# Kernel optimization log

Measured on AMD Instinct MI355X. Metric: run time of the kernel, lower is better.

## Reference

```python
import jax, jax.numpy as jnp
import numpy as np

B, T, N, H, L, KS = 8, 1024, 64, 8, 2, 3  # batch, seq_len, num_features(=graph n), heads, blocks, Cheb order
D1 = 64  # tq MLP hidden (hardcoded 64 in original)
EPS = 1e-6


def setup_inputs() -> dict:
    key = jax.random.key(0)
    ks = jax.random.split(key, 30)
    def nrm(k, shp, sc=0.05):
        return jax.random.normal(k, shp, dtype=jnp.float32) * sc
    return {
        "inputs": jax.random.normal(ks[0], (B, T, N), dtype=jnp.float32),
        "pos_emb": nrm(ks[1], (T, N)),
        "K3": nrm(ks[2], (N, KS, N), 0.1),  # Chebyshev kernel Lk reshaped [n, Ks, n] (constant)
        "qw": nrm(ks[3], (L, H, KS)), "qb": nrm(ks[4], (L, H)),
        "kw": nrm(ks[5], (L, H, KS)), "kb": nrm(ks[6], (L, H)),
        "vw": nrm(ks[7], (L, H, KS)), "vb": nrm(ks[8], (L, H)),
        "tqW1": nrm(ks[9], (L, H, T, D1)), "tqb1": nrm(ks[10], (L, H, D1)),
        "tqW2": nrm(ks[11], (L, H, D1, D1)), "tqb2": nrm(ks[12], (L, H, D1)),
        "tqW3": nrm(ks[13], (L, H, D1, 2)), "tqb3": nrm(ks[14], (L, H, 2)),
        "Wlt": nrm(ks[15], (L, H * N, N)),
        "ln1g": jnp.ones((L, N), jnp.float32), "ln1b": jnp.zeros((L, N), jnp.float32),
        "ln2g": jnp.ones((L, N), jnp.float32), "ln2b": jnp.zeros((L, N), jnp.float32),
        "sclw": nrm(ks[16], (L, KS)), "sclb": nrm(ks[17], (L,)),
        "elW": nrm(ks[18], (L, N, N)), "elb": nrm(ks[19], (L, N)),
        "fW1": nrm(ks[20], (N, 32)), "fb1": nrm(ks[21], (32,)),
        "fW2": nrm(ks[22], (32, 1)), "fb2": nrm(ks[23], (1,)),
    }


def _ln(x, g, b):
    m = jnp.mean(x, axis=-1, keepdims=True)
    v = jnp.mean((x - m) ** 2, axis=-1, keepdims=True)
    return (x - m) * jax.lax.rsqrt(v + EPS) * g + b


def _head_gconv(x, K3, ws, bs):
    # SpatialConvLayer (c_in=c_out=1) per head: relu(sum_k ws[h,k]*(x @ L_k) + bs[h] + x)
    g = jnp.einsum('btn,nkm,hk->bhtm', x, K3, ws) + bs[None, :, None, None]
    return jax.nn.relu(g + x[:, None])  # [B,H,T,N]


def reference(inputs, pos_emb, K3, qw, qb, kw, kb, vw, vb, tqW1, tqb1, tqW2, tqb2,
              tqW3, tqb3, Wlt, ln1g, ln1b, ln2g, ln2b, sclw, sclb, elW, elb,
              fW1, fb1, fW2, fb2):
    x = inputs + pos_emb  # position embedding layer
    for l in range(L):
        xq = _head_gconv(x, K3, qw[l], qb[l])
        xk = _head_gconv(x, K3, kw[l], kb[l])
        xv = _head_gconv(x, K3, vw[l], vb[l])
        # s_a[b,t,s] = sum_n xk[b,t,n] * xq[b,s,n], scaled by 1/num_features
        s = jnp.einsum('bhtn,bhsn->bhts', xk, xq) / N
        sft = jax.nn.softmax(s, axis=-1)
        # talking-quantity gate: MLP over rows of transposed softmax matrix
        p = jnp.swapaxes(sft, -1, -2)  # [B,H,T,T]
        h1 = jax.nn.relu(jnp.einsum('bhts,hsd->bhtd', p, tqW1[l]) + tqb1[l][None, :, None, :])
        h2 = jax.nn.relu(jnp.einsum('bhtd,hde->bhte', h1, tqW2[l]) + tqb2[l][None, :, None, :])
        g = jax.nn.softmax(jnp.einsum('bhtd,hde->bhte', h2, tqW3[l]) + tqb3[l][None, :, None, :], axis=-1)  # [B,H,T,2]
        auv = jnp.einsum('bhts,bhsn->bhtn', sft, xv)
        ho = g[..., 0:1] * auv + g[..., 1:2] * xv  # gated mix, [B,H,T,N]
        a_x = jnp.transpose(ho, (0, 2, 1, 3)).reshape(B, T, H * N)  # head concat
        out1 = _ln(x + a_x @ Wlt[l], ln1g[l], ln1b[l])  # dropout omitted (inference)
        gc = jnp.einsum('btn,nkm,k->btm', out1, K3, sclw[l]) + sclb[l]
        ffn = jax.nn.relu(gc + out1)  # SpatialConvLayer residual relu
        ffn = ffn @ elW[l] + elb[l]
        x = _ln(out1 + ffn, ln2g[l], ln2b[l])
    pooled = jnp.mean(x, axis=1)  # GlobalAveragePooling1D
    h = jax.nn.relu(pooled @ fW1 + fb1)
    return h @ fW2 + fb2  # [B,1]
```

## Files before the change

kernel.cpp:

```cpp
#include <hip/hip_runtime.h>

typedef __attribute__((ext_vector_type(8))) short short8;
typedef __attribute__((ext_vector_type(4))) float f32x4;

#define BB 8
#define TT 1024
#define NN 64
#define HH 8
#define LL 2
#define KSS 3
#define DD1 64
#define EPSV 1e-6f
#define LOG2E 1.4426950408889634f

#define MFMA16(a, b, c) __builtin_amdgcn_mfma_f32_16x16x32_bf16(a, b, c, 0, 0, 0)
#define BAR() __builtin_amdgcn_s_barrier()
#define WAIT_VM8() asm volatile("s_waitcnt vmcnt(8)" ::: "memory")
#define WAIT_VM2() asm volatile("s_waitcnt vmcnt(2)" ::: "memory")
#define WAIT_VM0() asm volatile("s_waitcnt vmcnt(0)" ::: "memory")
#define WAIT_LGKM0() asm volatile("s_waitcnt lgkmcnt(0)" ::: "memory")

__device__ __forceinline__ float exp2_(float x) { return __builtin_amdgcn_exp2f(x); }
__device__ __forceinline__ float log2_(float x) { return __builtin_amdgcn_logf(x); }

__device__ __forceinline__ void split1(float x, ushort& hi, ushort& lo) {
  uint u = __float_as_uint(x);
  hi = (ushort)(u >> 16);
  float hf = __uint_as_float(u & 0xffff0000u);
  lo = (ushort)(__float_as_uint(x - hf) >> 16);
}
__device__ __forceinline__ uint pack2(float a, float b, uint& lo) {
  uint ua = __float_as_uint(a), ub = __float_as_uint(b);
  float ra = __uint_as_float(ua & 0xffff0000u);
  float rb = __uint_as_float(ub & 0xffff0000u);
  lo = (__float_as_uint(a - ra) >> 16) | (__float_as_uint(b - rb) & 0xffff0000u);
  return (ua >> 16) | (ub & 0xffff0000u);
}
__device__ __forceinline__ uint pack2rhu(float a, float b) {
  uint ua = __float_as_uint(a) + 0x8000u;
  uint ub = __float_as_uint(b) + 0x8000u;
  return (ua >> 16) | (ub & 0xffff0000u);
}
__device__ __forceinline__ ushort f2bfr(float x) {
  union { float f; uint u; } v; v.f = x;
  uint r = (v.u + 0x7fffu + ((v.u >> 16) & 1u)) >> 16;
  return (ushort)r;
}
__device__ __forceinline__ float bf2f(ushort b) {
  union { uint u; float f; } v; v.u = ((uint)b) << 16; return v.f;
}

__device__ __forceinline__ void gl2lds16(const ushort* g, ushort* l) {
  __builtin_amdgcn_global_load_lds(
      (const __attribute__((address_space(1))) void*)g,
      (__attribute__((address_space(3))) void*)l, 16, 0, 0);
}
__device__ __forceinline__ void stage_async(ushort* __restrict__ s,
                                            const ushort* __restrict__ g,
                                            int stride, int tid) {
  int w = tid >> 6;
  int sub = (tid & 63) >> 3, c = tid & 7;
#pragma unroll
  for (int i = 0; i < 2; ++i) {
    int rb = (i * 4 + w) * 8;
    gl2lds16(g + (size_t)(rb + sub) * stride + ((c ^ sub) << 3), s + rb * 64);
  }
}
__device__ __forceinline__ short8 frag(const ushort* __restrict__ s, int row, int ch) {
  return *(const short8*)(s + row * 64 + ((ch ^ (row & 7)) << 3));
}
__device__ __forceinline__ void stage_q32(ushort* __restrict__ s,
                                          const ushort* __restrict__ g, int tid) {
  int w = tid >> 6;
  int sub = (tid & 63) >> 3, c = tid & 7;
  int rb = w * 8, r = rb + sub;
  gl2lds16(g + (size_t)r * 64 + ((c ^ (r & 7)) << 3), s + rb * 64);
}
__device__ __forceinline__ void stage_v32(ushort* __restrict__ s,
                                          const ushort* __restrict__ g, int tid) {
  int w = tid >> 6;
  int noff = (tid & 63) >> 2, c = tid & 3;
  int nb = w * 16, n = nb + noff;
  gl2lds16(g + (size_t)n * 1024 + ((c ^ ((n >> 1) & 3)) << 3), s + nb * 32);
}
__device__ __forceinline__ short8 frag32(const ushort* __restrict__ s, int row, int g) {
  return *(const short8*)(s + row * 32 + ((g ^ ((row >> 1) & 3)) << 3));
}


__global__ void k_addpos(const float* __restrict__ in, const float* __restrict__ pe,
                         float* __restrict__ x, int total) {
  int idx = blockIdx.x * 256 + threadIdx.x;
  if (idx < total) {
    int tn = idx & (TT * NN - 1);
    x[idx] = in[idx] + pe[tn];
  }
}

__global__ void k_k3s(const float* __restrict__ K3, const float* __restrict__ sclwl,
                      ushort* __restrict__ dh) {
  int idx = blockIdx.x * 256 + threadIdx.x;
  int n = idx >> 6, m = idx & 63;
  float v = K3[n * 192 + m] * sclwl[0] + K3[n * 192 + 64 + m] * sclwl[1] +
            K3[n * 192 + 128 + m] * sclwl[2];
  dh[m * 64 + n] = f2bfr(v);
}

__global__ __launch_bounds__(256) void k_tsplit(const float* __restrict__ src,
                                                ushort* __restrict__ dh) {
  __shared__ float st[64][65];
  int blk = blockIdx.x;
  int mat = blk >> 4, rt = blk & 15;
  int tid = threadIdx.x;
  size_t sbase = ((size_t)mat * TT + rt * 64) * 64;
#pragma unroll
  for (int i = 0; i < 4; ++i) {
    int idx = tid + i * 256;
    int r = idx >> 4, c4 = idx & 15;
    float4 v = *(const float4*)(src + sbase + r * 64 + c4 * 4);
    st[r][c4 * 4 + 0] = v.x; st[r][c4 * 4 + 1] = v.y;
    st[r][c4 * 4 + 2] = v.z; st[r][c4 * 4 + 3] = v.w;
  }
  __syncthreads();
  size_t obase = (size_t)mat * (64 * (size_t)TT) + rt * 64;
#pragma unroll
  for (int i = 0; i < 2; ++i) {
    int idx = tid + i * 256;
    int n = idx >> 3, c = idx & 7;
    uint hw[4];
#pragma unroll
    for (int j = 0; j < 4; ++j)
      hw[j] = (uint)f2bfr(st[c * 8 + 2 * j][n]) | ((uint)f2bfr(st[c * 8 + 2 * j + 1][n]) << 16);
    *(uint4*)(dh + obase + (size_t)n * TT + c * 8) = make_uint4(hw[0], hw[1], hw[2], hw[3]);
  }
}

__global__ __launch_bounds__(256) void k_tsplitW(const float* __restrict__ Wlt,
                                                 ushort* __restrict__ dh,
                                                 ushort* __restrict__ dl) {
  __shared__ float st[64][65];
  int blk = blockIdx.x;
  int l = blk >> 3, rt = blk & 7;
  int tid = threadIdx.x;
  size_t sbase = ((size_t)l * 512 + rt * 64) * 64;
#pragma unroll
  for (int i = 0; i < 4; ++i) {
    int idx = tid + i * 256;
    int r = idx >> 4, c4 = idx & 15;
    float4 v = *(const float4*)(Wlt + sbase + r * 64 + c4 * 4);
    st[r][c4 * 4 + 0] = v.x; st[r][c4 * 4 + 1] = v.y;
    st[r][c4 * 4 + 2] = v.z; st[r][c4 * 4 + 3] = v.w;
  }
  __syncthreads();
  size_t obase = (size_t)l * 64 * 512 + rt * 64;
#pragma unroll
  for (int i = 0; i < 2; ++i) {
    int idx = tid + i * 256;
    int n = idx >> 3, c = idx & 7;
    uint hw[4], lw[4];
#pragma unroll
    for (int j = 0; j < 4; ++j) hw[j] = pack2(st[c * 8 + 2 * j][n], st[c * 8 + 2 * j + 1][n], lw[j]);
    *(uint4*)(dh + obase + (size_t)n * 512 + c * 8) = make_uint4(hw[0], hw[1], hw[2], hw[3]);
    *(uint4*)(dl + obase + (size_t)n * 512 + c * 8) = make_uint4(lw[0], lw[1], lw[2], lw[3]);
  }
}

__global__ __launch_bounds__(256) void k_tsplitSq(const float* __restrict__ src,
                                                  ushort* __restrict__ dh) {
  __shared__ float st[64][65];
  int mat = blockIdx.x;
  int tid = threadIdx.x;
  size_t sbase = (size_t)mat * 4096;
#pragma unroll
  for (int i = 0; i < 4; ++i) {
    int idx = tid + i * 256;
    int r = idx >> 4, c4 = idx & 15;
    float4 v = *(const float4*)(src + sbase + r * 64 + c4 * 4);
    st[r][c4 * 4 + 0] = v.x; st[r][c4 * 4 + 1] = v.y;
    st[r][c4 * 4 + 2] = v.z; st[r][c4 * 4 + 3] = v.w;
  }
  __syncthreads();
#pragma unroll
  for (int i = 0; i < 2; ++i) {
    int idx = tid + i * 256;
    int d = idx >> 3, c = idx & 7;
    uint hw[4];
#pragma unroll
    for (int j = 0; j < 4; ++j)
      hw[j] = (uint)f2bfr(st[c * 8 + 2 * j][d]) | ((uint)f2bfr(st[c * 8 + 2 * j + 1][d]) << 16);
    *(uint4*)(dh + sbase + (size_t)d * 64 + c * 8) = make_uint4(hw[0], hw[1], hw[2], hw[3]);
  }
}

__global__ __launch_bounds__(256) void k_gconv(
    const float* __restrict__ x, const float* __restrict__ K3,
    const float* __restrict__ qwl, const float* __restrict__ qbl,
    const float* __restrict__ kwl, const float* __restrict__ kbl,
    const float* __restrict__ vwl, const float* __restrict__ vbl,
    ushort* __restrict__ xqh, ushort* __restrict__ xkh, float* __restrict__ xv) {
  __shared__ float sK3[12288];
  __shared__ float sx[4][64];
  int tid = threadIdx.x;
  int w = tid >> 6, lane = tid & 63;
#pragma unroll
  for (int i = 0; i < 12; ++i)
    ((float4*)sK3)[tid + i * 256] = ((const float4*)K3)[tid + i * 256];
  size_t bt = (size_t)blockIdx.x * 4 + w;
  size_t b = bt >> 10, t = bt & 1023;
  float xm = x[bt * 64 + lane];
  sx[w][lane] = xm;
  __syncthreads();
  float a0 = 0.f, a1 = 0.f, a2 = 0.f;
#pragma unroll 8
  for (int n = 0; n < 64; ++n) {
    float xn = sx[w][n];
    a0 = fmaf(xn, sK3[n * 192 + lane], a0);
    a1 = fmaf(xn, sK3[n * 192 + 64 + lane], a1);
    a2 = fmaf(xn, sK3[n * 192 + 128 + lane], a2);
  }
#pragma unroll
  for (int hh = 0; hh < HH; ++hh) {
    size_t off = (((size_t)b * HH + hh) * TT + t) * 64 + lane;
    float q = fmaf(qwl[hh * 3 + 0], a0,
              fmaf(qwl[hh * 3 + 1], a1, fmaf(qwl[hh * 3 + 2], a2, qbl[hh] + xm)));
    q = fmaxf(q, 0.f) * (0.015625f * LOG2E);
    xqh[off] = f2bfr(q);
    float k = fmaf(kwl[hh * 3 + 0], a0,
              fmaf(kwl[hh * 3 + 1], a1, fmaf(kwl[hh * 3 + 2], a2, kbl[hh] + xm)));
    xkh[off] = f2bfr(fmaxf(k, 0.f));
    float v = fmaf(vwl[hh * 3 + 0], a0,
              fmaf(vwl[hh * 3 + 1], a1, fmaf(vwl[hh * 3 + 2], a2, vbl[hh] + xm)));
    xv[off] = fmaxf(v, 0.f);
  }
}

__global__ __launch_bounds__(256, 4) void k_attn(
    const ushort* __restrict__ xkh, const ushort* __restrict__ xqh,
    const ushort* __restrict__ xvTh,
    float* __restrict__ auv, float* __restrict__ lse) {
  __shared__ ushort sQh[4096];
  __shared__ ushort sVh[4096];
  __shared__ ushort sPh[2048];
  int tid = threadIdx.x;
  int lane = tid & 63, w = tid >> 6;
  int l15 = lane & 15, g = lane >> 4;
  int nb = gridDim.x, chunk = nb >> 3, bid = blockIdx.x;
  int blk = (bid & 7) * chunk + (bid >> 3);
  int bh = blk >> 4, t0 = (blk & 15) << 6;
  size_t bhTT = (size_t)bh * TT;
  int trow = 16 * w + l15, psw = (trow >> 1) & 3;

  stage_async(sQh, xkh + (bhTT + t0) * NN, 64, tid);
  WAIT_VM0();
  BAR();
  short8 fKh[2];
#pragma unroll
  for (int ks = 0; ks < 2; ++ks) fKh[ks] = frag(sQh, trow, g + 4 * ks);
  WAIT_LGKM0();
  BAR();
  stage_q32(sQh, xqh + bhTT * NN, tid);
  stage_v32(sVh, xvTh + bhTT * NN, tid);
  stage_q32(sQh + 2048, xqh + (bhTT + 32) * NN, tid);
  stage_v32(sVh + 2048, xvTh + bhTT * NN + 32, tid);

  float lsum = 0.f;
  f32x4 O[4];
#pragma unroll
  for (int ct = 0; ct < 4; ++ct)
#pragma unroll
    for (int r = 0; r < 4; ++r) O[ct][r] = 0.f;

  for (int ut = 0; ut < 32; ++ut) {
    int cur = ut & 1;
    if (ut < 31) WAIT_VM2(); else WAIT_VM0();
    BAR();
    const ushort* cQh = sQh + cur * 2048;
    const ushort* cVh = sVh + cur * 2048;

    __builtin_amdgcn_s_setprio(1);
    f32x4 S[2];
#pragma unroll
    for (int rt = 0; rt < 2; ++rt) {
      f32x4 a = {0.f, 0.f, 0.f, 0.f};
#pragma unroll
      for (int ks = 0; ks < 2; ++ks)
        a = MFMA16(frag(cQh, 16 * rt + l15, g + 4 * ks), fKh[ks], a);
      S[rt] = a;
    }
    __builtin_amdgcn_s_setprio(0);

    uint2 ph[2];
#pragma unroll
    for (int rt = 0; rt < 2; ++rt) {
      float p0 = exp2_(S[rt][0]), p1 = exp2_(S[rt][1]);
      float p2 = exp2_(S[rt][2]), p3 = exp2_(S[rt][3]);
      lsum += (p0 + p1) + (p2 + p3);
      ph[rt].x = pack2rhu(p0, p1);
      ph[rt].y = pack2rhu(p2, p3);
    }
#pragma unroll
    for (int rt = 0; rt < 2; ++rt) {
      int ch = 2 * rt + (g >> 1);
      int off = trow * 32 + ((ch ^ psw) << 3) + ((g & 1) << 2);
      *(uint2*)(sPh + off) = ph[rt];
    }
    WAIT_LGKM0();
    __builtin_amdgcn_sched_barrier(0);
    __builtin_amdgcn_s_setprio(1);
    {
      short8 aPh = frag32(sPh, trow, g);
#pragma unroll
      for (int ct = 0; ct < 4; ++ct)
        O[ct] = MFMA16(aPh, frag32(cVh, 16 * ct + l15, g), O[ct]);
    }
    __builtin_amdgcn_s_setprio(0);
    WAIT_LGKM0();
    BAR();
    if (ut < 30) {
      int tn = ut + 2;
      stage_q32(sQh + cur * 2048, xqh + (bhTT + tn * 32) * NN, tid);
      stage_v32(sVh + cur * 2048, xvTh + bhTT * NN + tn * 32, tid);
    }
  }
  lsum += __shfl_xor(lsum, 16, 64);
  lsum += __shfl_xor(lsum, 32, 64);
  float il = 1.0f / lsum;
  float ilr[4];
#pragma unroll
  for (int r = 0; r < 4; ++r) ilr[r] = __shfl(il, (lane & 48) | (4 * g + r), 64);
#pragma unroll
  for (int r = 0; r < 4; ++r) {
    size_t row = (bhTT + t0 + 16 * w + 4 * g + r) * NN;
#pragma unroll
    for (int ct = 0; ct < 4; ++ct) auv[row + 16 * ct + l15] = O[ct][r] * ilr[r];
  }
  if (g == 0) lse[bhTT + t0 + trow] = log2_(lsum);
}

__global__ __launch_bounds__(256, 4) void k_h1(
    const ushort* __restrict__ xkh, const ushort* __restrict__ xqh,
    const ushort* __restrict__ w1Th,
    const float* __restrict__ lse, const float* __restrict__ b1,
    ushort* __restrict__ h1h) {
  __shared__ ushort sKh[4096];
  __shared__ ushort sWh[4096];
  __shared__ ushort sPh[2048];
  __shared__ float sL[1024];
  int tid = threadIdx.x;
  int lane = tid & 63, w = tid >> 6;
  int l15 = lane & 15, g = lane >> 4;
  int nb = gridDim.x, chunk = nb >> 3, bid = blockIdx.x;
  int blk = (bid & 7) * chunk + (bid >> 3);
  int bh = blk >> 4, h = bh & (HH - 1), a0 = (blk & 15) << 6;
  size_t bhTT = (size_t)bh * TT;
  size_t wbase = (size_t)h * NN * TT;
  int arow = 16 * w + l15, psw = (arow >> 1) & 3;

  stage_async(sKh, xqh + (bhTT + a0) * NN, 64, tid);
  WAIT_VM0();
  BAR();
  short8 fQh[2];
#pragma unroll
  for (int ks = 0; ks < 2; ++ks) fQh[ks] = frag(sKh, arow, g + 4 * ks);
#pragma unroll
  for (int i = 0; i < 4; ++i) sL[tid + i * 256] = lse[bhTT + tid + i * 256];
  WAIT_LGKM0();
  BAR();
  stage_q32(sKh, xkh + bhTT * NN, tid);
  stage_v32(sWh, w1Th + wbase, tid);
  stage_q32(sKh + 2048, xkh + (bhTT + 32) * NN, tid);
  stage_v32(sWh + 2048, w1Th + wbase + 32, tid);

  f32x4 acc[4];
#pragma unroll
  for (int ct = 0; ct < 4; ++ct)
#pragma unroll
    for (int r = 0; r < 4; ++r) acc[ct][r] = 0.f;

  for (int tt = 0; tt < 32; ++tt) {
    int cur = tt & 1;
    if (tt < 31) WAIT_VM2(); else WAIT_VM0();
    BAR();
    const ushort* cKh = sKh + cur * 2048;
    const ushort* cWh = sWh + cur * 2048;

    __builtin_amdgcn_s_setprio(1);
    f32x4 S[2];
#pragma unroll
    for (int rt = 0; rt < 2; ++rt) {
      f32x4 a = {0.f, 0.f, 0.f, 0.f};
#pragma unroll
      for (int ks = 0; ks < 2; ++ks)
        a = MFMA16(frag(cKh, 16 * rt + l15, g + 4 * ks), fQh[ks], a);
      S[rt] = a;
    }
    __builtin_amdgcn_s_setprio(0);

    uint2 ph[2];
#pragma unroll
    for (int rt = 0; rt < 2; ++rt) {
      f32x4 lv = *(const f32x4*)(sL + tt * 32 + 16 * rt + 4 * g);
      float p0 = exp2_(S[rt][0] - lv[0]);
      float p1 = exp2_(S[rt][1] - lv[1]);
      float p2 = exp2_(S[rt][2] - lv[2]);
      float p3 = exp2_(S[rt][3] - lv[3]);
      ph[rt].x = pack2rhu(p0, p1);
      ph[rt].y = pack2rhu(p2, p3);
    }
#pragma unroll
    for (int rt = 0; rt < 2; ++rt) {
      int ch = 2 * rt + (g >> 1);
      int off = arow * 32 + ((ch ^ psw) << 3) + ((g & 1) << 2);
      *(uint2*)(sPh + off) = ph[rt];
    }
    WAIT_LGKM0();
    __builtin_amdgcn_sched_barrier(0);
    __builtin_amdgcn_s_setprio(1);
    {
      short8 aPh = frag32(sPh, arow, g);
#pragma unroll
      for (int ct = 0; ct < 4; ++ct)
        acc[ct] = MFMA16(aPh, frag32(cWh, 16 * ct + l15, g), acc[ct]);
    }
    __builtin_amdgcn_s_setprio(0);
    WAIT_LGKM0();
    BAR();
    if (tt < 30) {
      int tn = tt + 2;
      stage_q32(sKh + cur * 2048, xkh + (bhTT + tn * 32) * NN, tid);
      stage_v32(sWh + cur * 2048, w1Th + wbase + tn * 32, tid);
    }
  }
#pragma unroll
  for (int ct = 0; ct < 4; ++ct) {
    float bb = b1[h * 64 + 16 * ct + l15];
#pragma unroll
    for (int r = 0; r < 4; ++r)
      h1h[(bhTT + a0 + 16 * w + 4 * g + r) * NN + 16 * ct + l15] =
          f2bfr(fmaxf(acc[ct][r] + bb, 0.f));
  }
}

__global__ __launch_bounds__(256) void k_gate(
    const ushort* __restrict__ h1h, const float* __restrict__ xv,
    const ushort* __restrict__ w2Th, const float* __restrict__ b2l,
    const float* __restrict__ W3l, const float* __restrict__ b3l,
    const float* __restrict__ auv, ushort* __restrict__ hoh,
    ushort* __restrict__ hol) {
  __shared__ ushort sA[4096], sB[4096];
  __shared__ float sred[2][64][4];
  __shared__ float sg[64][2];
  int tid = threadIdx.x;
  int lane = tid & 63, w = tid >> 6;
  int l15 = lane & 15, g = lane >> 4;
  int blk = blockIdx.x;
  int bh = blk >> 4, t0 = (blk & 15) << 6, h = bh & (HH - 1);
  size_t bhTT = (size_t)bh * TT;
  stage_async(sA, h1h + (bhTT + t0) * NN, 64, tid);
  stage_async(sB, w2Th + (size_t)h * 4096, 64, tid);
  WAIT_VM0();
  BAR();
  f32x4 acc[4];
#pragma unroll
  for (int rt = 0; rt < 4; ++rt)
#pragma unroll
    for (int r = 0; r < 4; ++r) acc[rt][r] = 0.f;
#pragma unroll
  for (int ks = 0; ks < 2; ++ks) {
    short8 bB = frag(sB, 16 * w + l15, g + 4 * ks);
#pragma unroll
    for (int rt = 0; rt < 4; ++rt)
      acc[rt] = MFMA16(frag(sA, 16 * rt + l15, g + 4 * ks), bB, acc[rt]);
  }
  int col = 16 * w + l15;
  float b2c = b2l[h * 64 + col];
  float w30 = W3l[h * 128 + col * 2 + 0];
  float w31 = W3l[h * 128 + col * 2 + 1];
#pragma unroll
  for (int rt = 0; rt < 4; ++rt)
#pragma unroll
    for (int r = 0; r < 4; ++r) {
      float v = fmaxf(acc[rt][r] + b2c, 0.f);
      float z0 = v * w30, z1 = v * w31;
#pragma unroll
      for (int mm = 1; mm < 16; mm <<= 1) {
        z0 += __shfl_xor(z0, mm, 64);
        z1 += __shfl_xor(z1, mm, 64);
      }
      if (l15 == 0) {
        int row = 16 * rt + 4 * g + r;
        sred[0][row][w] = z0;
        sred[1][row][w] = z1;
      }
    }
  __syncthreads();
  if (tid < 64) {
    float z0 = sred[0][tid][0] + sred[0][tid][1] + sred[0][tid][2] + sred[0][tid][3] +
               b3l[h * 2 + 0];
    float z1 = sred[1][tid][0] + sred[1][tid][1] + sred[1][tid][2] + sred[1][tid][3] +
               b3l[h * 2 + 1];
    float g0 = 1.0f / (1.0f + __expf(z1 - z0));
    sg[tid][0] = g0;
    sg[tid][1] = 1.0f - g0;
  }
  __syncthreads();
#pragma unroll
  for (int rr = 0; rr < 16; ++rr) {
    int row = 16 * w + rr;
    size_t off = (bhTT + t0 + row) * 64 + lane;
    float ho = sg[row][0] * auv[off] + sg[row][1] * xv[off];
    ushort hb, lb;
    split1(ho, hb, lb);
    hoh[off] = hb;
    hol[off] = lb;
  }
}

__global__ __launch_bounds__(256, 2) void k_merge(
    const float* __restrict__ x, const ushort* __restrict__ hoh,
    const ushort* __restrict__ hol, const ushort* __restrict__ wth,
    const ushort* __restrict__ wtl, const float* __restrict__ g1l,
    const float* __restrict__ b1l, ushort* __restrict__ out1h,
    ushort* __restrict__ out1l) {
  __shared__ ushort sAh[2][4096], sAl[2][4096], sBh[2][4096], sBl[2][4096];
  __shared__ float sred[2][64][4];
  __shared__ float sfin[64][2];
  int tid = threadIdx.x;
  int lane = tid & 63, w = tid >> 6;
  int l15 = lane & 15, g = lane >> 4;
  int blk = blockIdx.x;
  int b = blk >> 4, t0 = (blk & 15) << 6;

  {
    size_t ab0 = (((size_t)b * HH + 0) * TT + t0) * NN;
    size_t ab1 = (((size_t)b * HH + 1) * TT + t0) * NN;
    stage_async(sAh[0], hoh + ab0, 64, tid);
    stage_async(sAl[0], hol + ab0, 64, tid);
    stage_async(sBh[0], wth, 512, tid);
    stage_async(sBl[0], wtl, 512, tid);
    stage_async(sAh[1], hoh + ab1, 64, tid);
    stage_async(sAl[1], hol + ab1, 64, tid);
    stage_async(sBh[1], wth + 64, 512, tid);
    stage_async(sBl[1], wtl + 64, 512, tid);
  }

  f32x4 acc[4];
#pragma unroll
  for (int rt = 0; rt < 4; ++rt)
#pragma unroll
    for (int r = 0; r < 4; ++r) acc[rt][r] = 0.f;

  for (int h = 0; h < 8; ++h) {
    int cur = h & 1;
    if (h < 7) WAIT_VM8(); else WAIT_VM0();
    BAR();
    __builtin_amdgcn_s_setprio(1);
#pragma unroll
    for (int ks = 0; ks < 2; ++ks) {
      short8 bBh = frag(sBh[cur], 16 * w + l15, g + 4 * ks);
      short8 bBl = frag(sBl[cur], 16 * w + l15, g + 4 * ks);
#pragma unroll
      for (int rt = 0; rt < 4; ++rt) {
        short8 aAh = frag(sAh[cur], 16 * rt + l15, g + 4 * ks);
        short8 aAl = frag(sAl[cur], 16 * rt + l15, g + 4 * ks);
        acc[rt] = MFMA16(aAh, bBh, acc[rt]);
        acc[rt] = MFMA16(aAh, bBl, acc[rt]);
        acc[rt] = MFMA16(aAl, bBh, acc[rt]);
      }
    }
    __builtin_amdgcn_s_setprio(0);
    WAIT_LGKM0();
    BAR();
    if (h < 6) {
      int hn = h + 2;
      size_t ab = (((size_t)b * HH + hn) * TT + t0) * NN;
      stage_async(sAh[cur], hoh + ab, 64, tid);
      stage_async(sAl[cur], hol + ab, 64, tid);
      stage_async(sBh[cur], wth + hn * 64, 512, tid);
      stage_async(sBl[cur], wtl + hn * 64, 512, tid);
    }
  }
  int mcol = 16 * w + l15;
  float vv[4][4];
#pragma unroll
  for (int rt = 0; rt < 4; ++rt)
#pragma unroll
    for (int r = 0; r < 4; ++r) {
      int row = 16 * rt + 4 * g + r;
      vv[rt][r] = acc[rt][r] + x[((size_t)b * TT + t0 + row) * 64 + mcol];
    }
#pragma unroll
  for (int rt = 0; rt < 4; ++rt)
#pragma unroll
    for (int r = 0; r < 4; ++r) {
      float s1 = vv[rt][r], s2 = vv[rt][r] * vv[rt][r];
#pragma unroll
      for (int mm = 1; mm < 16; mm <<= 1) {
        s1 += __shfl_xor(s1, mm, 64);
        s2 += __shfl_xor(s2, mm, 64);
      }
      if (l15 == 0) {
        int row = 16 * rt + 4 * g + r;
        sred[0][row][w] = s1;
        sred[1][row][w] = s2;
      }
    }
  __syncthreads();
  if (tid < 64) {
    float a1 = sred[0][tid][0] + sred[0][tid][1] + sred[0][tid][2] + sred[0][tid][3];
    float a2 = sred[1][tid][0] + sred[1][tid][1] + sred[1][tid][2] + sred[1][tid][3];
    float mean = a1 * (1.0f / 64.0f);
    float var = a2 * (1.0f / 64.0f) - mean * mean;
    sfin[tid][0] = mean;
    sfin[tid][1] = rsqrtf(var + EPSV);
  }
  __syncthreads();
  float gg = g1l[mcol], bb = b1l[mcol];
#pragma unroll
  for (int rt = 0; rt < 4; ++rt)
#pragma unroll
    for (int r = 0; r < 4; ++r) {
      int row = 16 * rt + 4 * g + r;
      float mean = sfin[row][0], rstd = sfin[row][1];
      float val = (vv[rt][r] - mean) * rstd * gg + bb;
      ushort hb, lb;
      split1(val, hb, lb);
      size_t idx = ((size_t)b * TT + t0 + row) * 64 + mcol;
      out1h[idx] = hb;
      out1l[idx] = lb;
    }
}

__global__ __launch_bounds__(256) void k_ffn(
    const ushort* __restrict__ o1h_, const ushort* __restrict__ o1l_,
    const float* __restrict__ sclb_l, const ushort* __restrict__ k3sTh,
    const ushort* __restrict__ elWTh, const float* __restrict__ elbl,
    const float* __restrict__ g2l, const float* __restrict__ b2l,
    float* __restrict__ xout) {
  __shared__ ushort sAh[2048], sAl[2048];
  __shared__ ushort sB1[4096], sB2[4096];
  __shared__ float sred[2][32][4];
  __shared__ float sfin[32][2];
  int tid = threadIdx.x;
  int lane = tid & 63, w = tid >> 6;
  int l15 = lane & 15, g = lane >> 4;
  int blk = blockIdx.x;
  int b = blk >> 5, t0 = (blk & 31) << 5;
  size_t rb = ((size_t)b * TT + t0) * 64;

  stage_q32(sAh, o1h_ + rb, tid);
  stage_q32(sAl, o1l_ + rb, tid);
  stage_async(sB1, k3sTh, 64, tid);
  stage_async(sB2, elWTh, 64, tid);
  WAIT_VM0();
  BAR();

  int col = 16 * w + l15;
  f32x4 acc[2];
#pragma unroll
  for (int rt = 0; rt < 2; ++rt)
#pragma unroll
    for (int r = 0; r < 4; ++r) acc[rt][r] = 0.f;
#pragma unroll
  for (int ks = 0; ks < 2; ++ks) {
    short8 bB = frag(sB1, col, g + 4 * ks);
#pragma unroll
    for (int rt = 0; rt < 2; ++rt) {
      acc[rt] = MFMA16(frag(sAh, 16 * rt + l15, g + 4 * ks), bB, acc[rt]);
      acc[rt] = MFMA16(frag(sAl, 16 * rt + l15, g + 4 * ks), bB, acc[rt]);
    }
  }
  float sclb = sclb_l[0];
  int cch = col >> 3, cin = col & 7;
  float o1v[2][4], f1v[2][4];
#pragma unroll
  for (int rt = 0; rt < 2; ++rt)
#pragma unroll
    for (int r = 0; r < 4; ++r) {
      int row = 16 * rt + 4 * g + r;
      int a = row * 64 + (((cch ^ (row & 7)) << 3)) + cin;
      float o1 = bf2f(sAh[a]) + bf2f(sAl[a]);
      o1v[rt][r] = o1;
      f1v[rt][r] = fmaxf(acc[rt][r] + sclb + o1, 0.f);
    }
  __syncthreads();
#pragma unroll
  for (int rt = 0; rt < 2; ++rt)
#pragma unroll
    for (int r = 0; r < 4; ++r) {
      int row = 16 * rt + 4 * g + r;
      int a = row * 64 + (((cch ^ (row & 7)) << 3)) + cin;
      ushort hb, lb;
      split1(f1v[rt][r], hb, lb);
      sAh[a] = hb;
      sAl[a] = lb;
    }
  __syncthreads();
  f32x4 acc2[2];
#pragma unroll
  for (int rt = 0; rt < 2; ++rt)
#pragma unroll
    for (int r = 0; r < 4; ++r) acc2[rt][r] = 0.f;
#pragma unroll
  for (int ks = 0; ks < 2; ++ks) {
    short8 bB = frag(sB2, col, g + 4 * ks);
#pragma unroll
    for (int rt = 0; rt < 2; ++rt) {
      acc2[rt] = MFMA16(frag(sAh, 16 * rt + l15, g + 4 * ks), bB, acc2[rt]);
      acc2[rt] = MFMA16(frag(sAl, 16 * rt + l15, g + 4 * ks), bB, acc2[rt]);
    }
  }
  float elb = elbl[col];
  float vv[2][4];
#pragma unroll
  for (int rt = 0; rt < 2; ++rt)
#pragma unroll
    for (int r = 0; r < 4; ++r) {
      vv[rt][r] = o1v[rt][r] + acc2[rt][r] + elb;
      float s1 = vv[rt][r], s2 = vv[rt][r] * vv[rt][r];
#pragma unroll
      for (int mm = 1; mm < 16; mm <<= 1) {
        s1 += __shfl_xor(s1, mm, 64);
        s2 += __shfl_xor(s2, mm, 64);
      }
      if (l15 == 0) {
        int row = 16 * rt + 4 * g + r;
        sred[0][row][w] = s1;
        sred[1][row][w] = s2;
      }
    }
  __syncthreads();
  if (tid < 32) {
    float a1 = sred[0][tid][0] + sred[0][tid][1] + sred[0][tid][2] + sred[0][tid][3];
    float a2 = sred[1][tid][0] + sred[1][tid][1] + sred[1][tid][2] + sred[1][tid][3];
    float mean = a1 * (1.0f / 64.0f);
    float var = a2 * (1.0f / 64.0f) - mean * mean;
    sfin[tid][0] = mean;
    sfin[tid][1] = rsqrtf(var + EPSV);
  }
  __syncthreads();
  float gg = g2l[col], bb = b2l[col];
#pragma unroll
  for (int rt = 0; rt < 2; ++rt)
#pragma unroll
    for (int r = 0; r < 4; ++r) {
      int row = 16 * rt + 4 * g + r;
      xout[rb + (size_t)row * 64 + col] =
          (vv[rt][r] - sfin[row][0]) * sfin[row][1] * gg + bb;
    }
}

__global__ __launch_bounds__(256) void k_final(
    const float* __restrict__ x, const float* __restrict__ fW1,
    const float* __restrict__ fb1, const float* __restrict__ fW2,
    const float* __restrict__ fb2, float* __restrict__ out) {
  __shared__ float pl[4][64];
  int tid = threadIdx.x;
  int lane = tid & 63, w = tid >> 6;
  size_t b = blockIdx.x;
  float s = 0.f;
  for (int t = 256 * w; t < 256 * w + 256; ++t) s += x[(b * TT + t) * 64 + lane];
  pl[w][lane] = s;
  __syncthreads();
  if (tid < 64) pl[0][tid] = (pl[0][tid] + pl[1][tid] + pl[2][tid] + pl[3][tid]) * (1.0f / TT);
  __syncthreads();
  if (tid < 64) {
    float hv = 0.f;
    if (lane < 32) {
      hv = fb1[lane];
#pragma unroll 8
      for (int n = 0; n < 64; ++n) hv = fmaf(pl[0][n], fW1[n * 32 + lane], hv);
      hv = fmaxf(hv, 0.f) * fW2[lane];
    }
#pragma unroll
    for (int m = 1; m < 64; m <<= 1) hv += __shfl_xor(hv, m, 64);
    if (lane == 0) out[b] = hv + fb2[0];
  }
}

extern "C" void kernel_launch(void* const* d_in, const int* in_sizes, int n_in,
                              void* d_out, int out_size, void* d_ws, size_t ws_size,
                              hipStream_t stream) {
  const float* inputs = (const float*)d_in[0];
  const float* pos_emb = (const float*)d_in[1];
  const float* K3 = (const float*)d_in[2];
  const float* qw = (const float*)d_in[3];
  const float* qb = (const float*)d_in[4];
  const float* kw = (const float*)d_in[5];
  const float* kb = (const float*)d_in[6];
  const float* vw = (const float*)d_in[7];
  const float* vb = (const float*)d_in[8];
  const float* tqW1 = (const float*)d_in[9];
  const float* tqb1 = (const float*)d_in[10];
  const float* tqW2 = (const float*)d_in[11];
  const float* tqb2 = (const float*)d_in[12];
  const float* tqW3 = (const float*)d_in[13];
  const float* tqb3 = (const float*)d_in[14];
  const float* Wlt = (const float*)d_in[15];
  const float* ln1g = (const float*)d_in[16];
  const float* ln1b = (const float*)d_in[17];
  const float* ln2g = (const float*)d_in[18];
  const float* ln2b = (const float*)d_in[19];
  const float* sclw = (const float*)d_in[20];
  const float* sclb = (const float*)d_in[21];
  const float* elW = (const float*)d_in[22];
  const float* elb = (const float*)d_in[23];
  const float* fW1 = (const float*)d_in[24];
  const float* fb1 = (const float*)d_in[25];
  const float* fW2 = (const float*)d_in[26];
  const float* fb2 = (const float*)d_in[27];
  float* out = (float*)d_out;
  float* ws_f = (float*)d_ws;

  const size_t TN = (size_t)TT * NN;
  const size_t HTN = (size_t)HH * TT * NN;
  const size_t W1T_ELEMS = (size_t)LL * HH * NN * TT;
  const size_t WLT_ELEMS = (size_t)LL * 64 * 512;

  ushort* k3sTh = (ushort*)ws_f;
  ushort* w1Th = k3sTh + (size_t)LL * 4096;
  ushort* wth = w1Th + W1T_ELEMS;
  ushort* wtl = wth + WLT_ELEMS;
  ushort* w2Th = wtl + WLT_ELEMS;
  ushort* elWTh = w2Th + (size_t)LL * HH * 4096;
  size_t base_ush = (size_t)LL * 4096 + W1T_ELEMS + 2 * WLT_ELEMS +
                    (size_t)LL * HH * 4096 + (size_t)LL * 4096;
  const size_t base = (base_ush + 1) / 2;

  for (int l = 0; l < LL; ++l)
    k_k3s<<<16, 256, 0, stream>>>(K3, sclw + l * KSS, k3sTh + (size_t)l * 4096);
  k_tsplit<<<LL * HH * 16, 256, 0, stream>>>(tqW1, w1Th);
  k_tsplitW<<<LL * 8, 256, 0, stream>>>(Wlt, wth, wtl);
  k_tsplitSq<<<LL * HH, 256, 0, stream>>>(tqW2, w2Th);
  k_tsplitSq<<<LL, 256, 0, stream>>>(elW, elWTh);

  const size_t per_b = 2 * TN + (size_t)HH * TT + 5 * HTN;
  size_t avail = ws_size / sizeof(float);
  avail = (avail > base) ? avail - base : 0;
  int Bc = (int)(avail / per_b);
  if (Bc > BB) Bc = BB;
  if (Bc < 1) Bc = 1;

  for (int b0 = 0; b0 < BB; b0 += Bc) {
    int bc = (BB - b0 < Bc) ? (BB - b0) : Bc;
    float* x = ws_f + base;
    float* xv = x + (size_t)bc * TN;
    float* auv = xv + (size_t)bc * HTN;
    float* lseb = auv + (size_t)bc * HTN;
    ushort* out1h = (ushort*)(lseb + (size_t)bc * HH * TT);
    ushort* out1l = out1h + (size_t)bc * TN;
    ushort* h1h = out1l + (size_t)bc * TN;
    ushort* xqh = h1h + (size_t)bc * HTN;
    ushort* xkh = xqh + (size_t)bc * HTN;
    ushort* xvTh = xkh + (size_t)bc * HTN;
    ushort* hoh = xvTh + (size_t)bc * HTN;
    ushort* hol = hoh + (size_t)bc * HTN;

    int total = bc * (int)TN;
    k_addpos<<<(total + 255) / 256, 256, 0, stream>>>(inputs + (size_t)b0 * TN, pos_emb, x,
                                                      total);
    for (int l = 0; l < LL; ++l) {
      k_gconv<<<bc * TT / 4, 256, 0, stream>>>(x, K3, qw + l * HH * KSS, qb + l * HH,
                                               kw + l * HH * KSS, kb + l * HH,
                                               vw + l * HH * KSS, vb + l * HH,
                                               xqh, xkh, xv);
      k_tsplit<<<bc * HH * 16, 256, 0, stream>>>(xv, xvTh);
      k_attn<<<bc * HH * 16, 256, 0, stream>>>(xkh, xqh, xvTh, auv, lseb);
      k_h1<<<bc * HH * 16, 256, 0, stream>>>(
          xkh, xqh, w1Th + (size_t)l * HH * NN * TT, lseb,
          tqb1 + l * HH * DD1, h1h);
      k_gate<<<bc * HH * 16, 256, 0, stream>>>(
          h1h, xv, w2Th + (size_t)l * HH * 4096, tqb2 + l * HH * DD1,
          tqW3 + (size_t)l * HH * DD1 * 2, tqb3 + l * HH * 2, auv, hoh, hol);
      k_merge<<<bc * 16, 256, 0, stream>>>(x, hoh, hol, wth + (size_t)l * 64 * 512,
                                           wtl + (size_t)l * 64 * 512, ln1g + l * NN,
                                           ln1b + l * NN, out1h, out1l);
      k_ffn<<<bc * 32, 256, 0, stream>>>(out1h, out1l, sclb + l,
                                         k3sTh + (size_t)l * 4096,
                                         elWTh + (size_t)l * 4096, elb + l * NN,
                                         ln2g + l * NN, ln2b + l * NN, x);
    }
    k_final<<<bc, 256, 0, stream>>>(x, fW1, fb1, fW2, fb2, out + b0);
  }
}
```

Before: 261.6 us.

## Fuse gate MLP into h1 kernel and FFN into merge kernel

Folds the second and third MLP layers and the gated mix into the h1 kernel, so the h1 activations stay in shared memory and never go to global memory. Also folds the Chebyshev FFN, the dense layer and the second layernorm into the head-merge kernel, which keeps out1 in LDS instead of writing and re-reading split bf16 buffers. This cuts two launches per layer and their global round trips. In exchange the h1 kernel uses more LDS, which may lower occupancy. The FFN work now runs on 64-row tiles in only bc*16 blocks where it used 32-row tiles in bc*32 blocks.

```diff
diff --git a/kernel.cpp b/kernel.cpp
--- a/kernel.cpp
+++ b/kernel.cpp
@@ -337,14 +337,18 @@
   if (g == 0) lse[bhTT + t0 + trow] = log2_(lsum);
 }
 
-__global__ __launch_bounds__(256, 4) void k_h1(
+__global__ __launch_bounds__(256, 4) void k_h1g(
     const ushort* __restrict__ xkh, const ushort* __restrict__ xqh,
-    const ushort* __restrict__ w1Th,
-    const float* __restrict__ lse, const float* __restrict__ b1,
-    ushort* __restrict__ h1h) {
+    const ushort* __restrict__ w1Th, const float* __restrict__ lse,
+    const float* __restrict__ b1, const ushort* __restrict__ w2Th,
+    const float* __restrict__ b2l, const float* __restrict__ W3l,
+    const float* __restrict__ b3l, const float* __restrict__ auv,
+    const float* __restrict__ xv, ushort* __restrict__ hoh,
+    ushort* __restrict__ hol) {
   __shared__ ushort sKh[4096];
   __shared__ ushort sWh[4096];
   __shared__ ushort sPh[2048];
+  __shared__ ushort sW2[4096];
   __shared__ float sL[1024];
   int tid = threadIdx.x;
   int lane = tid & 63, w = tid >> 6;
@@ -357,6 +361,7 @@
   int arow = 16 * w + l15, psw = (arow >> 1) & 3;
 
   stage_async(sKh, xqh + (bhTT + a0) * NN, 64, tid);
+  stage_async(sW2, w2Th + (size_t)h * 4096, 64, tid);
   WAIT_VM0();
   BAR();
   short8 fQh[2];
@@ -434,53 +439,39 @@
 #pragma unroll
   for (int ct = 0; ct < 4; ++ct) {
     float bb = b1[h * 64 + 16 * ct + l15];
-#pragma unroll
-    for (int r = 0; r < 4; ++r)
-      h1h[(bhTT + a0 + 16 * w + 4 * g + r) * NN + 16 * ct + l15] =
-          f2bfr(fmaxf(acc[ct][r] + bb, 0.f));
-  }
-}
-
-__global__ __launch_bounds__(256) void k_gate(
-    const ushort* __restrict__ h1h, const float* __restrict__ xv,
-    const ushort* __restrict__ w2Th, const float* __restrict__ b2l,
-    const float* __restrict__ W3l, const float* __restrict__ b3l,
-    const float* __restrict__ auv, ushort* __restrict__ hoh,
-    ushort* __restrict__ hol) {
-  __shared__ ushort sA[4096], sB[4096];
-  __shared__ float sred[2][64][4];
-  __shared__ float sg[64][2];
-  int tid = threadIdx.x;
-  int lane = tid & 63, w = tid >> 6;
-  int l15 = lane & 15, g = lane >> 4;
-  int blk = blockIdx.x;
-  int bh = blk >> 4, t0 = (blk & 15) << 6, h = bh & (HH - 1);
-  size_t bhTT = (size_t)bh * TT;
-  stage_async(sA, h1h + (bhTT + t0) * NN, 64, tid);
-  stage_async(sB, w2Th + (size_t)h * 4096, 64, tid);
-  WAIT_VM0();
+    int cch = 2 * ct + (l15 >> 3), cin = l15 & 7;
+#pragma unroll
+    for (int r = 0; r < 4; ++r) {
+      int row = 16 * w + 4 * g + r;
+      float hv = fmaxf(acc[ct][r] + bb, 0.f);
+      sWh[row * 64 + ((cch ^ (row & 7)) << 3) + cin] = f2bfr(hv);
+    }
+  }
+  WAIT_LGKM0();
   BAR();
-  f32x4 acc[4];
-#pragma unroll
-  for (int rt = 0; rt < 4; ++rt)
-#pragma unroll
-    for (int r = 0; r < 4; ++r) acc[rt][r] = 0.f;
+  f32x4 acc2[4];
+#pragma unroll
+  for (int rt = 0; rt < 4; ++rt)
+#pragma unroll
+    for (int r = 0; r < 4; ++r) acc2[rt][r] = 0.f;
 #pragma unroll
   for (int ks = 0; ks < 2; ++ks) {
-    short8 bB = frag(sB, 16 * w + l15, g + 4 * ks);
+    short8 bB = frag(sW2, 16 * w + l15, g + 4 * ks);
 #pragma unroll
     for (int rt = 0; rt < 4; ++rt)
-      acc[rt] = MFMA16(frag(sA, 16 * rt + l15, g + 4 * ks), bB, acc[rt]);
+      acc2[rt] = MFMA16(frag(sWh, 16 * rt + l15, g + 4 * ks), bB, acc2[rt]);
   }
   int col = 16 * w + l15;
   float b2c = b2l[h * 64 + col];
   float w30 = W3l[h * 128 + col * 2 + 0];
   float w31 = W3l[h * 128 + col * 2 + 1];
+  float* sredf = sL;
+  float* sgf = sL + 512;
 #pragma unroll
   for (int rt = 0; rt < 4; ++rt)
 #pragma unroll
     for (int r = 0; r < 4; ++r) {
-      float v = fmaxf(acc[rt][r] + b2c, 0.f);
+      float v = fmaxf(acc2[rt][r] + b2c, 0.f);
       float z0 = v * w30, z1 = v * w31;
 #pragma unroll
       for (int mm = 1; mm < 16; mm <<= 1) {
@@ -489,26 +480,26 @@
       }
       if (l15 == 0) {
         int row = 16 * rt + 4 * g + r;
-        sred[0][row][w] = z0;
-        sred[1][row][w] = z1;
+        sredf[row * 4 + w] = z0;
+        sredf[256 + row * 4 + w] = z1;
       }
     }
   __syncthreads();
   if (tid < 64) {
-    float z0 = sred[0][tid][0] + sred[0][tid][1] + sred[0][tid][2] + sred[0][tid][3] +
-               b3l[h * 2 + 0];
-    float z1 = sred[1][tid][0] + sred[1][tid][1] + sred[1][tid][2] + sred[1][tid][3] +
-               b3l[h * 2 + 1];
+    float z0 = sredf[tid * 4] + sredf[tid * 4 + 1] + sredf[tid * 4 + 2] +
+               sredf[tid * 4 + 3] + b3l[h * 2 + 0];
+    float z1 = sredf[256 + tid * 4] + sredf[256 + tid * 4 + 1] +
+               sredf[256 + tid * 4 + 2] + sredf[256 + tid * 4 + 3] + b3l[h * 2 + 1];
     float g0 = 1.0f / (1.0f + __expf(z1 - z0));
-    sg[tid][0] = g0;
-    sg[tid][1] = 1.0f - g0;
+    sgf[tid * 2] = g0;
+    sgf[tid * 2 + 1] = 1.0f - g0;
   }
   __syncthreads();
 #pragma unroll
   for (int rr = 0; rr < 16; ++rr) {
     int row = 16 * w + rr;
-    size_t off = (bhTT + t0 + row) * 64 + lane;
-    float ho = sg[row][0] * auv[off] + sg[row][1] * xv[off];
+    size_t off = (bhTT + a0 + row) * 64 + lane;
+    float ho = sgf[row * 2] * auv[off] + sgf[row * 2 + 1] * xv[off];
     ushort hb, lb;
     split1(ho, hb, lb);
     hoh[off] = hb;
@@ -516,12 +507,14 @@
   }
 }
 
-__global__ __launch_bounds__(256, 2) void k_merge(
-    const float* __restrict__ x, const ushort* __restrict__ hoh,
+__global__ __launch_bounds__(256, 2) void k_mrgf(
+    float* __restrict__ x, const ushort* __restrict__ hoh,
     const ushort* __restrict__ hol, const ushort* __restrict__ wth,
     const ushort* __restrict__ wtl, const float* __restrict__ g1l,
-    const float* __restrict__ b1l, ushort* __restrict__ out1h,
-    ushort* __restrict__ out1l) {
+    const float* __restrict__ b1l, const float* __restrict__ sclb_l,
+    const ushort* __restrict__ k3sTh, const ushort* __restrict__ elWTh,
+    const float* __restrict__ elbl, const float* __restrict__ g2l,
+    const float* __restrict__ b2l) {
   __shared__ ushort sAh[2][4096], sAl[2][4096], sBh[2][4096], sBl[2][4096];
   __shared__ float sred[2][64][4];
   __shared__ float sfin[64][2];
@@ -580,6 +573,8 @@
       stage_async(sBl[cur], wtl + hn * 64, 512, tid);
     }
   }
+  stage_async(sBh[0], k3sTh, 64, tid);
+  stage_async(sBl[0], elWTh, 64, tid);
   int mcol = 16 * w + l15;
   float vv[4][4];
 #pragma unroll
@@ -615,109 +610,80 @@
     sfin[tid][1] = rsqrtf(var + EPSV);
   }
   __syncthreads();
-  float gg = g1l[mcol], bb = b1l[mcol];
+  float gg = g1l[mcol], bb1 = b1l[mcol];
+  float val[4][4];
+  ushort* sH = sAh[0];
+  ushort* sHl = sAl[0];
+  int cch = mcol >> 3, cin = mcol & 7;
 #pragma unroll
   for (int rt = 0; rt < 4; ++rt)
 #pragma unroll
     for (int r = 0; r < 4; ++r) {
       int row = 16 * rt + 4 * g + r;
-      float mean = sfin[row][0], rstd = sfin[row][1];
-      float val = (vv[rt][r] - mean) * rstd * gg + bb;
+      float v = (vv[rt][r] - sfin[row][0]) * sfin[row][1] * gg + bb1;
+      val[rt][r] = v;
       ushort hb, lb;
-      split1(val, hb, lb);
-      size_t idx = ((size_t)b * TT + t0 + row) * 64 + mcol;
-      out1h[idx] = hb;
-      out1l[idx] = lb;
-    }
-}
-
-__global__ __launch_bounds__(256) void k_ffn(
-    const ushort* __restrict__ o1h_, const ushort* __restrict__ o1l_,
-    const float* __restrict__ sclb_l, const ushort* __restrict__ k3sTh,
-    const ushort* __restrict__ elWTh, const float* __restrict__ elbl,
-    const float* __restrict__ g2l, const float* __restrict__ b2l,
-    float* __restrict__ xout) {
-  __shared__ ushort sAh[2048], sAl[2048];
-  __shared__ ushort sB1[4096], sB2[4096];
-  __shared__ float sred[2][32][4];
-  __shared__ float sfin[32][2];
-  int tid = threadIdx.x;
-  int lane = tid & 63, w = tid >> 6;
-  int l15 = lane & 15, g = lane >> 4;
-  int blk = blockIdx.x;
-  int b = blk >> 5, t0 = (blk & 31) << 5;
-  size_t rb = ((size_t)b * TT + t0) * 64;
-
-  stage_q32(sAh, o1h_ + rb, tid);
-  stage_q32(sAl, o1l_ + rb, tid);
-  stage_async(sB1, k3sTh, 64, tid);
-  stage_async(sB2, elWTh, 64, tid);
+      split1(v, hb, lb);
+      int a = row * 64 + ((cch ^ (row & 7)) << 3) + cin;
+      sH[a] = hb;
+      sHl[a] = lb;
+    }
   WAIT_VM0();
+  WAIT_LGKM0();
   BAR();
-
-  int col = 16 * w + l15;
-  f32x4 acc[2];
-#pragma unroll
-  for (int rt = 0; rt < 2; ++rt)
-#pragma unroll
-    for (int r = 0; r < 4; ++r) acc[rt][r] = 0.f;
+  f32x4 acc3[4];
+#pragma unroll
+  for (int rt = 0; rt < 4; ++rt)
+#pragma unroll
+    for (int r = 0; r < 4; ++r) acc3[rt][r] = 0.f;
 #pragma unroll
   for (int ks = 0; ks < 2; ++ks) {
-    short8 bB = frag(sB1, col, g + 4 * ks);
-#pragma unroll
-    for (int rt = 0; rt < 2; ++rt) {
-      acc[rt] = MFMA16(frag(sAh, 16 * rt + l15, g + 4 * ks), bB, acc[rt]);
-      acc[rt] = MFMA16(frag(sAl, 16 * rt + l15, g + 4 * ks), bB, acc[rt]);
-    }
-  }
+    short8 bB = frag(sBh[0], mcol, g + 4 * ks);
+#pragma unroll
+    for (int rt = 0; rt < 4; ++rt) {
+      acc3[rt] = MFMA16(frag(sH, 16 * rt + l15, g + 4 * ks), bB, acc3[rt]);
+      acc3[rt] = MFMA16(frag(sHl, 16 * rt + l15, g + 4 * ks), bB, acc3[rt]);
+    }
+  }
+  WAIT_LGKM0();
+  BAR();
   float sclb = sclb_l[0];
-  int cch = col >> 3, cin = col & 7;
-  float o1v[2][4], f1v[2][4];
-#pragma unroll
-  for (int rt = 0; rt < 2; ++rt)
+#pragma unroll
+  for (int rt = 0; rt < 4; ++rt)
 #pragma unroll
     for (int r = 0; r < 4; ++r) {
       int row = 16 * rt + 4 * g + r;
-      int a = row * 64 + (((cch ^ (row & 7)) << 3)) + cin;
-      float o1 = bf2f(sAh[a]) + bf2f(sAl[a]);
-      o1v[rt][r] = o1;
-      f1v[rt][r] = fmaxf(acc[rt][r] + sclb + o1, 0.f);
-    }
-  __syncthreads();
-#pragma unroll
-  for (int rt = 0; rt < 2; ++rt)
+      float f1 = fmaxf(acc3[rt][r] + sclb + val[rt][r], 0.f);
+      ushort hb, lb;
+      split1(f1, hb, lb);
+      int a = row * 64 + ((cch ^ (row & 7)) << 3) + cin;
+      sH[a] = hb;
+      sHl[a] = lb;
+    }
+  WAIT_LGKM0();
+  BAR();
+  f32x4 acc4[4];
+#pragma unroll
+  for (int rt = 0; rt < 4; ++rt)
+#pragma unroll
+    for (int r = 0; r < 4; ++r) acc4[rt][r] = 0.f;
+#pragma unroll
+  for (int ks = 0; ks < 2; ++ks) {
+    short8 bB = frag(sBl[0], mcol, g + 4 * ks);
+#pragma unroll
+    for (int rt = 0; rt < 4; ++rt) {
+      acc4[rt] = MFMA16(frag(sH, 16 * rt + l15, g + 4 * ks), bB, acc4[rt]);
+      acc4[rt] = MFMA16(frag(sHl, 16 * rt + l15, g + 4 * ks), bB, acc4[rt]);
+    }
+  }
+  float elb = elbl[mcol];
+#pragma unroll
+  for (int rt = 0; rt < 4; ++rt)
 #pragma unroll
     for (int r = 0; r < 4; ++r) {
-      int row = 16 * rt + 4 * g + r;
-      int a = row * 64 + (((cch ^ (row & 7)) << 3)) + cin;
-      ushort hb, lb;
-      split1(f1v[rt][r], hb, lb);
-      sAh[a] = hb;
-      sAl[a] = lb;
-    }
-  __syncthreads();
-  f32x4 acc2[2];
-#pragma unroll
-  for (int rt = 0; rt < 2; ++rt)
-#pragma unroll
-    for (int r = 0; r < 4; ++r) acc2[rt][r] = 0.f;
-#pragma unroll
-  for (int ks = 0; ks < 2; ++ks) {
-    short8 bB = frag(sB2, col, g + 4 * ks);
-#pragma unroll
-    for (int rt = 0; rt < 2; ++rt) {
-      acc2[rt] = MFMA16(frag(sAh, 16 * rt + l15, g + 4 * ks), bB, acc2[rt]);
-      acc2[rt] = MFMA16(frag(sAl, 16 * rt + l15, g + 4 * ks), bB, acc2[rt]);
-    }
-  }
-  float elb = elbl[col];
-  float vv[2][4];
-#pragma unroll
-  for (int rt = 0; rt < 2; ++rt)
-#pragma unroll
-    for (int r = 0; r < 4; ++r) {
-      vv[rt][r] = o1v[rt][r] + acc2[rt][r] + elb;
-      float s1 = vv[rt][r], s2 = vv[rt][r] * vv[rt][r];
+      float v = val[rt][r] + acc4[rt][r] + elb;
+      vv[rt][r] = v;
+      float s1 = v, s2 = v * v;
 #pragma unroll
       for (int mm = 1; mm < 16; mm <<= 1) {
         s1 += __shfl_xor(s1, mm, 64);
@@ -730,7 +696,7 @@
       }
     }
   __syncthreads();
-  if (tid < 32) {
+  if (tid < 64) {
     float a1 = sred[0][tid][0] + sred[0][tid][1] + sred[0][tid][2] + sred[0][tid][3];
     float a2 = sred[1][tid][0] + sred[1][tid][1] + sred[1][tid][2] + sred[1][tid][3];
     float mean = a1 * (1.0f / 64.0f);
@@ -739,14 +705,14 @@
     sfin[tid][1] = rsqrtf(var + EPSV);
   }
   __syncthreads();
-  float gg = g2l[col], bb = b2l[col];
-#pragma unroll
-  for (int rt = 0; rt < 2; ++rt)
+  float g2 = g2l[mcol], bb2 = b2l[mcol];
+#pragma unroll
+  for (int rt = 0; rt < 4; ++rt)
 #pragma unroll
     for (int r = 0; r < 4; ++r) {
       int row = 16 * rt + 4 * g + r;
-      xout[rb + (size_t)row * 64 + col] =
-          (vv[rt][r] - sfin[row][0]) * sfin[row][1] * gg + bb;
+      x[((size_t)b * TT + t0 + row) * 64 + mcol] =
+          (vv[rt][r] - sfin[row][0]) * sfin[row][1] * g2 + bb2;
     }
 }
 
@@ -834,7 +800,7 @@
   k_tsplitSq<<<LL * HH, 256, 0, stream>>>(tqW2, w2Th);
   k_tsplitSq<<<LL, 256, 0, stream>>>(elW, elWTh);
 
-  const size_t per_b = 2 * TN + (size_t)HH * TT + 5 * HTN;
+  const size_t per_b = TN + 2 * HTN + (size_t)HH * TT + (5 * HTN) / 2;
   size_t avail = ws_size / sizeof(float);
   avail = (avail > base) ? avail - base : 0;
   int Bc = (int)(avail / per_b);
@@ -847,10 +813,7 @@
     float* xv = x + (size_t)bc * TN;
     float* auv = xv + (size_t)bc * HTN;
     float* lseb = auv + (size_t)bc * HTN;
-    ushort* out1h = (ushort*)(lseb + (size_t)bc * HH * TT);
-    ushort* out1l = out1h + (size_t)bc * TN;
-    ushort* h1h = out1l + (size_t)bc * TN;
-    ushort* xqh = h1h + (size_t)bc * HTN;
+    ushort* xqh = (ushort*)(lseb + (size_t)bc * HH * TT);
     ushort* xkh = xqh + (size_t)bc * HTN;
     ushort* xvTh = xkh + (size_t)bc * HTN;
     ushort* hoh = xvTh + (size_t)bc * HTN;
@@ -866,19 +829,14 @@
                                                xqh, xkh, xv);
       k_tsplit<<<bc * HH * 16, 256, 0, stream>>>(xv, xvTh);
       k_attn<<<bc * HH * 16, 256, 0, stream>>>(xkh, xqh, xvTh, auv, lseb);
-      k_h1<<<bc * HH * 16, 256, 0, stream>>>(
-          xkh, xqh, w1Th + (size_t)l * HH * NN * TT, lseb,
-          tqb1 + l * HH * DD1, h1h);
-      k_gate<<<bc * HH * 16, 256, 0, stream>>>(
-          h1h, xv, w2Th + (size_t)l * HH * 4096, tqb2 + l * HH * DD1,
-          tqW3 + (size_t)l * HH * DD1 * 2, tqb3 + l * HH * 2, auv, hoh, hol);
-      k_merge<<<bc * 16, 256, 0, stream>>>(x, hoh, hol, wth + (size_t)l * 64 * 512,
-                                           wtl + (size_t)l * 64 * 512, ln1g + l * NN,
-                                           ln1b + l * NN, out1h, out1l);
-      k_ffn<<<bc * 32, 256, 0, stream>>>(out1h, out1l, sclb + l,
-                                         k3sTh + (size_t)l * 4096,
-                                         elWTh + (size_t)l * 4096, elb + l * NN,
-                                         ln2g + l * NN, ln2b + l * NN, x);
+      k_h1g<<<bc * HH * 16, 256, 0, stream>>>(
+          xkh, xqh, w1Th + (size_t)l * HH * NN * TT, lseb, tqb1 + l * HH * DD1,
+          w2Th + (size_t)l * HH * 4096, tqb2 + l * HH * DD1,
+          tqW3 + (size_t)l * HH * DD1 * 2, tqb3 + l * HH * 2, auv, xv, hoh, hol);
+      k_mrgf<<<bc * 16, 256, 0, stream>>>(
+          x, hoh, hol, wth + (size_t)l * 64 * 512, wtl + (size_t)l * 64 * 512,
+          ln1g + l * NN, ln1b + l * NN, sclb + l, k3sTh + (size_t)l * 4096,
+          elWTh + (size_t)l * 4096, elb + l * NN, ln2g + l * NN, ln2b + l * NN);
     }
     k_final<<<bc, 256, 0, stream>>>(x, fW1, fb1, fW2, fb2, out + b0);
   }
```

New measurement: 245.7 us. 6.1% less time.
